# Kernel tuning notes

Hardware: AMD Instinct MI355X
Metric: run time of the kernel (lower is better)

Reference implementation:

```python
import jax, jax.numpy as jnp
import numpy as np

EMBED_DIM = 512
NUM_HEADS = 8
HEAD_DIM = EMBED_DIM // NUM_HEADS


def setup_inputs() -> dict:
    key = jax.random.key(0)
    ks = jax.random.split(key, 9)
    d = EMBED_DIM
    s = 1.0 / np.sqrt(d)
    inp = {
        "x": jax.random.normal(ks[0], (2, 4096, d), dtype=jnp.float32),
        # torch nn.Linear weights are [out, in]; we store them the same way
        "Wq": jax.random.uniform(ks[1], (d, d), jnp.float32, -s, s),
        "bq": jax.random.uniform(ks[2], (d,), jnp.float32, -s, s),
        "Wk": jax.random.uniform(ks[3], (d, d), jnp.float32, -s, s),
        "bk": jax.random.uniform(ks[4], (d,), jnp.float32, -s, s),
        "Wv": jax.random.uniform(ks[5], (d, d), jnp.float32, -s, s),
        "bv": jax.random.uniform(ks[6], (d,), jnp.float32, -s, s),
        "Wo": jax.random.uniform(ks[7], (d, d), jnp.float32, -s, s),
        "bo": jax.random.uniform(ks[8], (d,), jnp.float32, -s, s),
    }
    return inp


def reference(x, Wq, bq, Wk, bk, Wv, bv, Wo, bo):
    B, S, D = x.shape
    H, Hd = NUM_HEADS, HEAD_DIM

    def proj(W, b):  # torch Linear: x @ W.T + b
        y = jnp.einsum("bsd,ed->bse", x, W) + b
        return y.reshape(B, S, H, Hd).transpose(0, 2, 1, 3)  # [B,H,S,Hd]

    Q = proj(Wq, bq)
    K = proj(Wk, bk)
    V = proj(Wv, bv)

    scale = 1.0 / jnp.sqrt(jnp.float32(Hd))
    scores = jnp.einsum("bhqd,bhkd->bhqk", Q, K) * scale  # [B,H,S,S]
    attn = jax.nn.softmax(scores, axis=-1)
    out = jnp.einsum("bhqk,bhkd->bhqd", attn, V)  # [B,H,S,Hd]
    out = out.transpose(0, 2, 1, 3).reshape(B, S, D)
    return jnp.einsum("bsd,ed->bse", out, Wo) + bo
```

## Files before the change

kernel.cpp:

```cpp
#include <hip/hip_runtime.h>


typedef unsigned short ushortT;
typedef __attribute__((ext_vector_type(8))) short short8;
typedef __attribute__((ext_vector_type(4))) float f32x4;
typedef __attribute__((ext_vector_type(16))) float f32x16;
typedef __attribute__((ext_vector_type(4))) unsigned int uint4v;
typedef __attribute__((ext_vector_type(2))) unsigned int uint2v;

__device__ __forceinline__ ushortT f2bf(float f) {
    unsigned int u = __builtin_bit_cast(unsigned int, f);
    u += 0x7FFFu + ((u >> 16) & 1u);
    return (ushortT)(u >> 16);
}

__device__ __forceinline__ unsigned int cvtpk(float lo, float hi) {
    unsigned int d;
    asm("v_cvt_pk_bf16_f32 %0, %1, %2" : "=v"(d) : "v"(lo), "v"(hi));
    return d;
}

__device__ __forceinline__ void plswap(unsigned int &a, unsigned int &b) {
    uint2v r = __builtin_amdgcn_permlane32_swap(a, b, false, false);
    a = r[0]; b = r[1];
}

#define GLDA 40
#define ALDK 72

__device__ __forceinline__ void stage_f32(ushortT* lds, const float* src)
{
    f32x4 a0 = *(const f32x4*)(src);
    f32x4 a1 = *(const f32x4*)(src + 4);
    short8 s;
    s[0] = (short)f2bf(a0[0]); s[1] = (short)f2bf(a0[1]);
    s[2] = (short)f2bf(a0[2]); s[3] = (short)f2bf(a0[3]);
    s[4] = (short)f2bf(a1[0]); s[5] = (short)f2bf(a1[1]);
    s[6] = (short)f2bf(a1[2]); s[7] = (short)f2bf(a1[3]);
    *(short8*)lds = s;
}

__global__ __launch_bounds__(256) void proj_qkv(
    const float* __restrict__ x,
    const float* __restrict__ Wq, const float* __restrict__ bq,
    const float* __restrict__ Wk, const float* __restrict__ bk,
    const float* __restrict__ Wv, const float* __restrict__ bv,
    ushortT* __restrict__ Qw, ushortT* __restrict__ Kw,
    ushortT* __restrict__ Vtw, float qscale)
{
    __shared__ __align__(16) ushortT As[128 * GLDA];
    __shared__ __align__(16) ushortT Bs[128 * GLDA];
    const int t = threadIdx.x;
    const int w = t >> 6, lane = t & 63;
    const int quad = lane >> 4, l15 = lane & 15;
    const int z = blockIdx.z;
    const int bx = blockIdx.x, by = blockIdx.y;
    const int wm = (w >> 1) * 64, wn = (w & 1) * 64;

    const float* W    = (z == 0) ? Wq : (z == 1) ? Wk : Wv;
    const float* bias = (z == 0) ? bq : (z == 1) ? bk : bv;
    const float* Asrc = (z < 2) ? x : W;
    const float* Bsrc = (z < 2) ? W : x;
    const int arow0 = (z < 2) ? bx * 128 : by * 128;
    const int brow0 = (z < 2) ? by * 128 : bx * 128;

    f32x4 acc[4][4] = {};

    for (int k0 = 0; k0 < 512; k0 += 32) {
#pragma unroll
        for (int i = 0; i < 2; i++) {
            int c = t + i * 256;
            int row = c >> 2, cc = c & 3;
            stage_f32(As + row * GLDA + cc * 8,
                      Asrc + (size_t)(arow0 + row) * 512 + k0 + cc * 8);
            stage_f32(Bs + row * GLDA + cc * 8,
                      Bsrc + (size_t)(brow0 + row) * 512 + k0 + cc * 8);
        }
        __syncthreads();
        short8 af[4], bfr[4];
#pragma unroll
        for (int i = 0; i < 4; i++)
            af[i] = *(const short8*)(As + (wm + i * 16 + l15) * GLDA + quad * 8);
#pragma unroll
        for (int i = 0; i < 4; i++)
            bfr[i] = *(const short8*)(Bs + (wn + i * 16 + l15) * GLDA + quad * 8);
#pragma unroll
        for (int mi = 0; mi < 4; mi++)
#pragma unroll
            for (int ni = 0; ni < 4; ni++)
                acc[mi][ni] = __builtin_amdgcn_mfma_f32_16x16x32_bf16(
                    af[mi], bfr[ni], acc[mi][ni], 0, 0, 0);
        __syncthreads();
    }

    if (z < 2) {
        ushortT* Y = (z == 0) ? Qw : Kw;
        const float sc = (z == 0) ? qscale : 1.0f;
#pragma unroll
        for (int ni = 0; ni < 4; ni++) {
            int col = brow0 + wn + ni * 16 + l15;
            float bv_ = bias[col];
#pragma unroll
            for (int mi = 0; mi < 4; mi++)
#pragma unroll
                for (int r = 0; r < 4; r++) {
                    int row = arow0 + wm + mi * 16 + quad * 4 + r;
                    Y[(size_t)row * 512 + col] = f2bf((acc[mi][ni][r] + bv_) * sc);
                }
        }
    } else {
        const int bidx = brow0 >> 12;
        const int s0 = brow0 & 4095;
#pragma unroll
        for (int mi = 0; mi < 4; mi++)
#pragma unroll
            for (int r = 0; r < 4; r++) {
                int ch = arow0 + wm + mi * 16 + quad * 4 + r;
                float bv_ = bias[ch];
#pragma unroll
                for (int ni = 0; ni < 4; ni++) {
                    int s = s0 + wn + ni * 16 + l15;
                    Vtw[(size_t)bidx * 2097152 + (size_t)ch * 4096 + s] =
                        f2bf(acc[mi][ni][r] + bv_);
                }
            }
    }
}

__global__ __launch_bounds__(256) void gemm_out(
    const ushortT* __restrict__ X, const float* __restrict__ W,
    const float* __restrict__ bias, float* __restrict__ Y)
{
    __shared__ __align__(16) ushortT As[128 * GLDA];
    __shared__ __align__(16) ushortT Bs[128 * GLDA];
    const int t = threadIdx.x;
    const int w = t >> 6, lane = t & 63;
    const int quad = lane >> 4, l15 = lane & 15;
    const int bm = blockIdx.x * 128, bn = blockIdx.y * 128;
    const int wm = (w >> 1) * 64, wn = (w & 1) * 64;

    f32x4 acc[4][4] = {};

    for (int k0 = 0; k0 < 512; k0 += 32) {
#pragma unroll
        for (int i = 0; i < 2; i++) {
            int c = t + i * 256;
            int row = c >> 2, cc = c & 3;
            *(uint4v*)(As + row * GLDA + cc * 8) =
                *(const uint4v*)(X + (size_t)(bm + row) * 512 + k0 + cc * 8);
            stage_f32(Bs + row * GLDA + cc * 8,
                      W + (size_t)(bn + row) * 512 + k0 + cc * 8);
        }
        __syncthreads();
        short8 af[4], bfr[4];
#pragma unroll
        for (int i = 0; i < 4; i++)
            af[i] = *(const short8*)(As + (wm + i * 16 + l15) * GLDA + quad * 8);
#pragma unroll
        for (int i = 0; i < 4; i++)
            bfr[i] = *(const short8*)(Bs + (wn + i * 16 + l15) * GLDA + quad * 8);
#pragma unroll
        for (int mi = 0; mi < 4; mi++)
#pragma unroll
            for (int ni = 0; ni < 4; ni++)
                acc[mi][ni] = __builtin_amdgcn_mfma_f32_16x16x32_bf16(
                    af[mi], bfr[ni], acc[mi][ni], 0, 0, 0);
        __syncthreads();
    }

#pragma unroll
    for (int ni = 0; ni < 4; ni++) {
        int col = bn + wn + ni * 16 + l15;
        float bv = bias[col];
#pragma unroll
        for (int mi = 0; mi < 4; mi++)
#pragma unroll
            for (int r = 0; r < 4; r++) {
                int row = bm + wm + mi * 16 + quad * 4 + r;
                Y[(size_t)row * 512 + col] = acc[mi][ni][r] + bv;
            }
    }
}

__global__ __launch_bounds__(512) void attn(
    const ushortT* Q, const ushortT* __restrict__ K,
    const ushortT* __restrict__ Vt, ushortT* O)
{
    __shared__ __align__(16) ushortT Ks[2][2][64 * ALDK];
    __shared__ __align__(16) ushortT Vs[2][2][64 * ALDK];

    const int t = threadIdx.x;
    const int w = t >> 6, lane = t & 63;
    const int half = w >> 2, wq = w & 3;
    const int l31 = lane & 31, hh = lane >> 5;
    const int qt = blockIdx.x, bh = blockIdx.y;
    const int b = bh >> 3, h = bh & 7;
    const size_t qrow = (size_t)b * 4096 + qt * 128 + wq * 32 + l31;

    short8 qf[4];
    {
        const ushortT* qp = Q + qrow * 512 + h * 64 + hh * 8;
#pragma unroll
        for (int dk = 0; dk < 4; dk++)
            qf[dk] = *(const short8*)(qp + dk * 16);
    }

    f32x16 oacc[2] = {};
    float lpart = 0.f;

    const int kofs = half * 2048;
    const ushortT* Kbase = K + ((size_t)b * 4096 + kofs) * 512 + h * 64;
    const ushortT* Vbase = Vt + (size_t)b * 2097152 + (size_t)h * 64 * 4096 + kofs;

    const int th = t & 255;
    const int srow = th >> 3, scol = (th & 7) * 8;
    uint4v kg[2], vg[2];

#pragma unroll
    for (int i = 0; i < 2; i++) {
        kg[i] = *(const uint4v*)(Kbase + (size_t)(srow + 32 * i) * 512 + scol);
        vg[i] = *(const uint4v*)(Vbase + (size_t)(srow + 32 * i) * 4096 + scol);
    }
#pragma unroll
    for (int i = 0; i < 2; i++) {
        *(uint4v*)(Ks[half][0] + (srow + 32 * i) * ALDK + scol) = kg[i];
        *(uint4v*)(Vs[half][0] + (srow + 32 * i) * ALDK + scol) = vg[i];
    }
    __syncthreads();

    for (int kt = 0; kt < 32; kt++) {
        const int cur = kt & 1;

        if (kt < 31) {
            const int kb = (kt + 1) * 64;
#pragma unroll
            for (int i = 0; i < 2; i++) {
                kg[i] = *(const uint4v*)(Kbase + (size_t)(kb + srow + 32 * i) * 512 + scol);
                vg[i] = *(const uint4v*)(Vbase + (size_t)(srow + 32 * i) * 4096 + kb + scol);
            }
        }

        const ushortT* Kt = Ks[half][cur];
        const ushortT* Vtl = Vs[half][cur];

#pragma unroll
        for (int st = 0; st < 2; st++) {
            f32x16 sacc = {};
#pragma unroll
            for (int dk = 0; dk < 4; dk++) {
                short8 kf = *(const short8*)(Kt + (st * 32 + l31) * ALDK + dk * 16 + hh * 8);
                sacc = __builtin_amdgcn_mfma_f32_32x32x16_bf16(kf, qf[dk], sacc, 0, 0, 0);
            }
            float p[16];
#pragma unroll
            for (int r = 0; r < 16; r++) {
                p[r] = __builtin_amdgcn_exp2f(sacc[r]);
                lpart += p[r];
            }
            unsigned int c00 = cvtpk(p[0],  p[1]),  c01 = cvtpk(p[2],  p[3]);
            unsigned int c10 = cvtpk(p[4],  p[5]),  c11 = cvtpk(p[6],  p[7]);
            unsigned int c20 = cvtpk(p[8],  p[9]),  c21 = cvtpk(p[10], p[11]);
            unsigned int c30 = cvtpk(p[12], p[13]), c31 = cvtpk(p[14], p[15]);
            plswap(c00, c10);
            plswap(c01, c11);
            plswap(c20, c30);
            plswap(c21, c31);
            uint4v b0v = { c00, c01, c10, c11 };
            uint4v b1v = { c20, c21, c30, c31 };
            short8 B0 = __builtin_bit_cast(short8, b0v);
            short8 B1 = __builtin_bit_cast(short8, b1v);

#pragma unroll
            for (int dt = 0; dt < 2; dt++) {
                short8 vf0 = *(const short8*)(Vtl + (dt * 32 + l31) * ALDK + st * 32 + hh * 8);
                short8 vf1 = *(const short8*)(Vtl + (dt * 32 + l31) * ALDK + st * 32 + 16 + hh * 8);
                oacc[dt] = __builtin_amdgcn_mfma_f32_32x32x16_bf16(vf0, B0, oacc[dt], 0, 0, 0);
                oacc[dt] = __builtin_amdgcn_mfma_f32_32x32x16_bf16(vf1, B1, oacc[dt], 0, 0, 0);
            }
        }

        if (kt < 31) {
            const int nb = cur ^ 1;
#pragma unroll
            for (int i = 0; i < 2; i++) {
                *(uint4v*)(Ks[half][nb] + (srow + 32 * i) * ALDK + scol) = kg[i];
                *(uint4v*)(Vs[half][nb] + (srow + 32 * i) * ALDK + scol) = vg[i];
            }
        }
        __syncthreads();
    }

    float* scratch = (float*)&Ks[0][0][0];
    float* prow = scratch + (size_t)(wq * 64 + lane) * 36;

    if (half == 1) {
#pragma unroll
        for (int dt = 0; dt < 2; dt++)
#pragma unroll
            for (int m = 0; m < 4; m++) {
                f32x4 v4 = { oacc[dt][4 * m + 0], oacc[dt][4 * m + 1],
                             oacc[dt][4 * m + 2], oacc[dt][4 * m + 3] };
                *(f32x4*)(prow + dt * 16 + m * 4) = v4;
            }
        prow[32] = lpart;
    }
    __syncthreads();

    if (half == 0) {
        float sum = lpart + prow[32];
        float l = sum + __shfl_xor(sum, 32);
        float rl = 1.0f / l;

        ushortT* orow = O + qrow * 512 + h * 64 + hh * 4;
#pragma unroll
        for (int dt = 0; dt < 2; dt++)
#pragma unroll
            for (int m = 0; m < 4; m++) {
                f32x4 v4 = *(const f32x4*)(prow + dt * 16 + m * 4);
                unsigned int u0 = cvtpk((oacc[dt][4 * m + 0] + v4[0]) * rl,
                                        (oacc[dt][4 * m + 1] + v4[1]) * rl);
                unsigned int u1 = cvtpk((oacc[dt][4 * m + 2] + v4[2]) * rl,
                                        (oacc[dt][4 * m + 3] + v4[3]) * rl);
                uint2v st2 = { u0, u1 };
                *(uint2v*)(orow + dt * 32 + m * 8) = st2;
            }
    }
}

extern "C" void kernel_launch(void* const* d_in, const int* in_sizes, int n_in,
                              void* d_out, int out_size, void* d_ws, size_t ws_size,
                              hipStream_t stream)
{
    const float* x  = (const float*)d_in[0];
    const float* Wq = (const float*)d_in[1];
    const float* bq = (const float*)d_in[2];
    const float* Wk = (const float*)d_in[3];
    const float* bk = (const float*)d_in[4];
    const float* Wv = (const float*)d_in[5];
    const float* bv = (const float*)d_in[6];
    const float* Wo = (const float*)d_in[7];
    const float* bo = (const float*)d_in[8];

    ushortT* ws  = (ushortT*)d_ws;
    ushortT* Qw  = ws;
    ushortT* Kw  = ws + 4194304;
    ushortT* Vtw = ws + 2 * 4194304;

    const float qscale = 0.125f * 1.44269504089f;

    proj_qkv<<<dim3(64, 4, 3), 256, 0, stream>>>(
        x, Wq, bq, Wk, bk, Wv, bv, Qw, Kw, Vtw, qscale);
    attn<<<dim3(32, 16), 512, 0, stream>>>(Qw, Kw, Vtw, Qw);
    gemm_out<<<dim3(64, 4), 256, 0, stream>>>(Qw, Wo, bo, (float*)d_out);
}
```

Measured before the change: 218.6 us.

## Double query rows per attention wave and register-prefetch GEMM staging loads

The attention kernel now gives each wave 64 query rows (two 32-row groups), so every K/V fragment read from LDS feeds twice as many MFMAs, and the grid is halved to 16x16 blocks. Launch bounds are set to request two blocks per CU, and the merge scratch is widened to hold both groups. The projection and output GEMMs prefetch the next k-tile's global loads into registers while the current tile computes, and use packed bf16 conversion instructions instead of scalar rounding. The costs are much higher register pressure in attention, possible spills or lower occupancy, and only 256 attention blocks, which may underfill the GPU.

```diff
diff --git a/kernel.cpp b/kernel.cpp
--- a/kernel.cpp
+++ b/kernel.cpp
@@ -20,6 +20,12 @@
     return d;
 }
 
+__device__ __forceinline__ uint4v pk8(f32x4 a0, f32x4 a1) {
+    uint4v r = { cvtpk(a0[0], a0[1]), cvtpk(a0[2], a0[3]),
+                 cvtpk(a1[0], a1[1]), cvtpk(a1[2], a1[3]) };
+    return r;
+}
+
 __device__ __forceinline__ void plswap(unsigned int &a, unsigned int &b) {
     uint2v r = __builtin_amdgcn_permlane32_swap(a, b, false, false);
     a = r[0]; b = r[1];
@@ -27,18 +33,6 @@
 
 #define GLDA 40
 #define ALDK 72
-
-__device__ __forceinline__ void stage_f32(ushortT* lds, const float* src)
-{
-    f32x4 a0 = *(const f32x4*)(src);
-    f32x4 a1 = *(const f32x4*)(src + 4);
-    short8 s;
-    s[0] = (short)f2bf(a0[0]); s[1] = (short)f2bf(a0[1]);
-    s[2] = (short)f2bf(a0[2]); s[3] = (short)f2bf(a0[3]);
-    s[4] = (short)f2bf(a1[0]); s[5] = (short)f2bf(a1[1]);
-    s[6] = (short)f2bf(a1[2]); s[7] = (short)f2bf(a1[3]);
-    *(short8*)lds = s;
-}
 
 __global__ __launch_bounds__(256) void proj_qkv(
     const float* __restrict__ x,
@@ -64,19 +58,42 @@
     const int arow0 = (z < 2) ? bx * 128 : by * 128;
     const int brow0 = (z < 2) ? by * 128 : bx * 128;
 
+    const int sr0 = t >> 2, sc0 = (t & 3) * 8;
+    const int sr1 = (t + 256) >> 2, sc1 = ((t + 256) & 3) * 8;
+
+    f32x4 pa[2][2], pb[2][2];
+    {
+        const float* ap0 = Asrc + (size_t)(arow0 + sr0) * 512 + sc0;
+        const float* ap1 = Asrc + (size_t)(arow0 + sr1) * 512 + sc1;
+        const float* bp0 = Bsrc + (size_t)(brow0 + sr0) * 512 + sc0;
+        const float* bp1 = Bsrc + (size_t)(brow0 + sr1) * 512 + sc1;
+        pa[0][0] = *(const f32x4*)ap0; pa[0][1] = *(const f32x4*)(ap0 + 4);
+        pa[1][0] = *(const f32x4*)ap1; pa[1][1] = *(const f32x4*)(ap1 + 4);
+        pb[0][0] = *(const f32x4*)bp0; pb[0][1] = *(const f32x4*)(bp0 + 4);
+        pb[1][0] = *(const f32x4*)bp1; pb[1][1] = *(const f32x4*)(bp1 + 4);
+    }
+
     f32x4 acc[4][4] = {};
 
     for (int k0 = 0; k0 < 512; k0 += 32) {
-#pragma unroll
-        for (int i = 0; i < 2; i++) {
-            int c = t + i * 256;
-            int row = c >> 2, cc = c & 3;
-            stage_f32(As + row * GLDA + cc * 8,
-                      Asrc + (size_t)(arow0 + row) * 512 + k0 + cc * 8);
-            stage_f32(Bs + row * GLDA + cc * 8,
-                      Bsrc + (size_t)(brow0 + row) * 512 + k0 + cc * 8);
-        }
+        *(uint4v*)(As + sr0 * GLDA + sc0) = pk8(pa[0][0], pa[0][1]);
+        *(uint4v*)(As + sr1 * GLDA + sc1) = pk8(pa[1][0], pa[1][1]);
+        *(uint4v*)(Bs + sr0 * GLDA + sc0) = pk8(pb[0][0], pb[0][1]);
+        *(uint4v*)(Bs + sr1 * GLDA + sc1) = pk8(pb[1][0], pb[1][1]);
         __syncthreads();
+
+        if (k0 < 480) {
+            const int kn = k0 + 32;
+            const float* ap0 = Asrc + (size_t)(arow0 + sr0) * 512 + kn + sc0;
+            const float* ap1 = Asrc + (size_t)(arow0 + sr1) * 512 + kn + sc1;
+            const float* bp0 = Bsrc + (size_t)(brow0 + sr0) * 512 + kn + sc0;
+            const float* bp1 = Bsrc + (size_t)(brow0 + sr1) * 512 + kn + sc1;
+            pa[0][0] = *(const f32x4*)ap0; pa[0][1] = *(const f32x4*)(ap0 + 4);
+            pa[1][0] = *(const f32x4*)ap1; pa[1][1] = *(const f32x4*)(ap1 + 4);
+            pb[0][0] = *(const f32x4*)bp0; pb[0][1] = *(const f32x4*)(bp0 + 4);
+            pb[1][0] = *(const f32x4*)bp1; pb[1][1] = *(const f32x4*)(bp1 + 4);
+        }
+
         short8 af[4], bfr[4];
 #pragma unroll
         for (int i = 0; i < 4; i++)
@@ -139,19 +156,39 @@
     const int bm = blockIdx.x * 128, bn = blockIdx.y * 128;
     const int wm = (w >> 1) * 64, wn = (w & 1) * 64;
 
+    const int sr0 = t >> 2, sc0 = (t & 3) * 8;
+    const int sr1 = (t + 256) >> 2, sc1 = ((t + 256) & 3) * 8;
+
+    uint4v pa[2];
+    f32x4 pb[2][2];
+    {
+        pa[0] = *(const uint4v*)(X + (size_t)(bm + sr0) * 512 + sc0);
+        pa[1] = *(const uint4v*)(X + (size_t)(bm + sr1) * 512 + sc1);
+        const float* bp0 = W + (size_t)(bn + sr0) * 512 + sc0;
+        const float* bp1 = W + (size_t)(bn + sr1) * 512 + sc1;
+        pb[0][0] = *(const f32x4*)bp0; pb[0][1] = *(const f32x4*)(bp0 + 4);
+        pb[1][0] = *(const f32x4*)bp1; pb[1][1] = *(const f32x4*)(bp1 + 4);
+    }
+
     f32x4 acc[4][4] = {};
 
     for (int k0 = 0; k0 < 512; k0 += 32) {
-#pragma unroll
-        for (int i = 0; i < 2; i++) {
-            int c = t + i * 256;
-            int row = c >> 2, cc = c & 3;
-            *(uint4v*)(As + row * GLDA + cc * 8) =
-                *(const uint4v*)(X + (size_t)(bm + row) * 512 + k0 + cc * 8);
-            stage_f32(Bs + row * GLDA + cc * 8,
-                      W + (size_t)(bn + row) * 512 + k0 + cc * 8);
-        }
+        *(uint4v*)(As + sr0 * GLDA + sc0) = pa[0];
+        *(uint4v*)(As + sr1 * GLDA + sc1) = pa[1];
+        *(uint4v*)(Bs + sr0 * GLDA + sc0) = pk8(pb[0][0], pb[0][1]);
+        *(uint4v*)(Bs + sr1 * GLDA + sc1) = pk8(pb[1][0], pb[1][1]);
         __syncthreads();
+
+        if (k0 < 480) {
+            const int kn = k0 + 32;
+            pa[0] = *(const uint4v*)(X + (size_t)(bm + sr0) * 512 + kn + sc0);
+            pa[1] = *(const uint4v*)(X + (size_t)(bm + sr1) * 512 + kn + sc1);
+            const float* bp0 = W + (size_t)(bn + sr0) * 512 + kn + sc0;
+            const float* bp1 = W + (size_t)(bn + sr1) * 512 + kn + sc1;
+            pb[0][0] = *(const f32x4*)bp0; pb[0][1] = *(const f32x4*)(bp0 + 4);
+            pb[1][0] = *(const f32x4*)bp1; pb[1][1] = *(const f32x4*)(bp1 + 4);
+        }
+
         short8 af[4], bfr[4];
 #pragma unroll
         for (int i = 0; i < 4; i++)
@@ -182,31 +219,52 @@
     }
 }
 
-__global__ __launch_bounds__(512) void attn(
+__device__ __forceinline__ void softmax_pack(const f32x16 &sacc, float &lp,
+                                             uint4v &B0, uint4v &B1)
+{
+    float p[16];
+#pragma unroll
+    for (int r = 0; r < 16; r++) {
+        p[r] = __builtin_amdgcn_exp2f(sacc[r]);
+        lp += p[r];
+    }
+    unsigned int c00 = cvtpk(p[0],  p[1]),  c01 = cvtpk(p[2],  p[3]);
+    unsigned int c10 = cvtpk(p[4],  p[5]),  c11 = cvtpk(p[6],  p[7]);
+    unsigned int c20 = cvtpk(p[8],  p[9]),  c21 = cvtpk(p[10], p[11]);
+    unsigned int c30 = cvtpk(p[12], p[13]), c31 = cvtpk(p[14], p[15]);
+    plswap(c00, c10);
+    plswap(c01, c11);
+    plswap(c20, c30);
+    plswap(c21, c31);
+    B0 = uint4v{ c00, c01, c10, c11 };
+    B1 = uint4v{ c20, c21, c30, c31 };
+}
+
+__global__ __launch_bounds__(512, 2) void attn(
     const ushortT* Q, const ushortT* __restrict__ K,
     const ushortT* __restrict__ Vt, ushortT* O)
 {
-    __shared__ __align__(16) ushortT Ks[2][2][64 * ALDK];
-    __shared__ __align__(16) ushortT Vs[2][2][64 * ALDK];
+    __shared__ __align__(16) ushortT SM[2][2][2][64 * ALDK];
 
     const int t = threadIdx.x;
     const int w = t >> 6, lane = t & 63;
-    const int half = w >> 2, wq = w & 3;
+    const int half = w >> 2, qw = w & 3;
     const int l31 = lane & 31, hh = lane >> 5;
     const int qt = blockIdx.x, bh = blockIdx.y;
     const int b = bh >> 3, h = bh & 7;
-    const size_t qrow = (size_t)b * 4096 + qt * 128 + wq * 32 + l31;
-
-    short8 qf[4];
-    {
-        const ushortT* qp = Q + qrow * 512 + h * 64 + hh * 8;
+    const size_t qbase = (size_t)b * 4096 + qt * 256 + qw * 64;
+
+    short8 qf[2][4];
+#pragma unroll
+    for (int qg = 0; qg < 2; qg++) {
+        const ushortT* qp = Q + (qbase + qg * 32 + l31) * 512 + h * 64 + hh * 8;
 #pragma unroll
         for (int dk = 0; dk < 4; dk++)
-            qf[dk] = *(const short8*)(qp + dk * 16);
-    }
-
-    f32x16 oacc[2] = {};
-    float lpart = 0.f;
+            qf[qg][dk] = *(const short8*)(qp + dk * 16);
+    }
+
+    f32x16 oacc[2][2] = {};
+    float lpart[2] = {};
 
     const int kofs = half * 2048;
     const ushortT* Kbase = K + ((size_t)b * 4096 + kofs) * 512 + h * 64;
@@ -223,8 +281,8 @@
     }
 #pragma unroll
     for (int i = 0; i < 2; i++) {
-        *(uint4v*)(Ks[half][0] + (srow + 32 * i) * ALDK + scol) = kg[i];
-        *(uint4v*)(Vs[half][0] + (srow + 32 * i) * ALDK + scol) = vg[i];
+        *(uint4v*)(SM[0][half][0] + (srow + 32 * i) * ALDK + scol) = kg[i];
+        *(uint4v*)(SM[1][half][0] + (srow + 32 * i) * ALDK + scol) = vg[i];
     }
     __syncthreads();
 
@@ -240,42 +298,38 @@
             }
         }
 
-        const ushortT* Kt = Ks[half][cur];
-        const ushortT* Vtl = Vs[half][cur];
+        const ushortT* Kt  = SM[0][half][cur];
+        const ushortT* Vtl = SM[1][half][cur];
 
 #pragma unroll
         for (int st = 0; st < 2; st++) {
-            f32x16 sacc = {};
+            short8 kf[4];
+#pragma unroll
+            for (int dk = 0; dk < 4; dk++)
+                kf[dk] = *(const short8*)(Kt + (st * 32 + l31) * ALDK + dk * 16 + hh * 8);
+            f32x16 s0 = {}, s1 = {};
 #pragma unroll
             for (int dk = 0; dk < 4; dk++) {
-                short8 kf = *(const short8*)(Kt + (st * 32 + l31) * ALDK + dk * 16 + hh * 8);
-                sacc = __builtin_amdgcn_mfma_f32_32x32x16_bf16(kf, qf[dk], sacc, 0, 0, 0);
-            }
-            float p[16];
-#pragma unroll
-            for (int r = 0; r < 16; r++) {
-                p[r] = __builtin_amdgcn_exp2f(sacc[r]);
-                lpart += p[r];
-            }
-            unsigned int c00 = cvtpk(p[0],  p[1]),  c01 = cvtpk(p[2],  p[3]);
-            unsigned int c10 = cvtpk(p[4],  p[5]),  c11 = cvtpk(p[6],  p[7]);
-            unsigned int c20 = cvtpk(p[8],  p[9]),  c21 = cvtpk(p[10], p[11]);
-            unsigned int c30 = cvtpk(p[12], p[13]), c31 = cvtpk(p[14], p[15]);
-            plswap(c00, c10);
-            plswap(c01, c11);
-            plswap(c20, c30);
-            plswap(c21, c31);
-            uint4v b0v = { c00, c01, c10, c11 };
-            uint4v b1v = { c20, c21, c30, c31 };
-            short8 B0 = __builtin_bit_cast(short8, b0v);
-            short8 B1 = __builtin_bit_cast(short8, b1v);
+                s0 = __builtin_amdgcn_mfma_f32_32x32x16_bf16(kf[dk], qf[0][dk], s0, 0, 0, 0);
+                s1 = __builtin_amdgcn_mfma_f32_32x32x16_bf16(kf[dk], qf[1][dk], s1, 0, 0, 0);
+            }
+
+            uint4v B00, B01, B10, B11;
+            softmax_pack(s0, lpart[0], B00, B01);
+            softmax_pack(s1, lpart[1], B10, B11);
+            short8 p00 = __builtin_bit_cast(short8, B00);
+            short8 p01 = __builtin_bit_cast(short8, B01);
+            short8 p10 = __builtin_bit_cast(short8, B10);
+            short8 p11 = __builtin_bit_cast(short8, B11);
 
 #pragma unroll
             for (int dt = 0; dt < 2; dt++) {
                 short8 vf0 = *(const short8*)(Vtl + (dt * 32 + l31) * ALDK + st * 32 + hh * 8);
                 short8 vf1 = *(const short8*)(Vtl + (dt * 32 + l31) * ALDK + st * 32 + 16 + hh * 8);
-                oacc[dt] = __builtin_amdgcn_mfma_f32_32x32x16_bf16(vf0, B0, oacc[dt], 0, 0, 0);
-                oacc[dt] = __builtin_amdgcn_mfma_f32_32x32x16_bf16(vf1, B1, oacc[dt], 0, 0, 0);
+                oacc[0][dt] = __builtin_amdgcn_mfma_f32_32x32x16_bf16(vf0, p00, oacc[0][dt], 0, 0, 0);
+                oacc[0][dt] = __builtin_amdgcn_mfma_f32_32x32x16_bf16(vf1, p01, oacc[0][dt], 0, 0, 0);
+                oacc[1][dt] = __builtin_amdgcn_mfma_f32_32x32x16_bf16(vf0, p10, oacc[1][dt], 0, 0, 0);
+                oacc[1][dt] = __builtin_amdgcn_mfma_f32_32x32x16_bf16(vf1, p11, oacc[1][dt], 0, 0, 0);
             }
         }
 
@@ -283,47 +337,53 @@
             const int nb = cur ^ 1;
 #pragma unroll
             for (int i = 0; i < 2; i++) {
-                *(uint4v*)(Ks[half][nb] + (srow + 32 * i) * ALDK + scol) = kg[i];
-                *(uint4v*)(Vs[half][nb] + (srow + 32 * i) * ALDK + scol) = vg[i];
+                *(uint4v*)(SM[0][half][nb] + (srow + 32 * i) * ALDK + scol) = kg[i];
+                *(uint4v*)(SM[1][half][nb] + (srow + 32 * i) * ALDK + scol) = vg[i];
             }
         }
         __syncthreads();
     }
 
-    float* scratch = (float*)&Ks[0][0][0];
-    float* prow = scratch + (size_t)(wq * 64 + lane) * 36;
+    float* scratch = (float*)&SM[0][0][0][0];
+    float* prow = scratch + (size_t)(qw * 64 + lane) * 68;
 
     if (half == 1) {
 #pragma unroll
-        for (int dt = 0; dt < 2; dt++)
-#pragma unroll
-            for (int m = 0; m < 4; m++) {
-                f32x4 v4 = { oacc[dt][4 * m + 0], oacc[dt][4 * m + 1],
-                             oacc[dt][4 * m + 2], oacc[dt][4 * m + 3] };
-                *(f32x4*)(prow + dt * 16 + m * 4) = v4;
-            }
-        prow[32] = lpart;
+        for (int qg = 0; qg < 2; qg++)
+#pragma unroll
+            for (int dt = 0; dt < 2; dt++)
+#pragma unroll
+                for (int m = 0; m < 4; m++) {
+                    f32x4 v4 = { oacc[qg][dt][4 * m + 0], oacc[qg][dt][4 * m + 1],
+                                 oacc[qg][dt][4 * m + 2], oacc[qg][dt][4 * m + 3] };
+                    *(f32x4*)(prow + qg * 32 + dt * 16 + m * 4) = v4;
+                }
+        prow[64] = lpart[0];
+        prow[65] = lpart[1];
     }
     __syncthreads();
 
     if (half == 0) {
-        float sum = lpart + prow[32];
-        float l = sum + __shfl_xor(sum, 32);
-        float rl = 1.0f / l;
-
-        ushortT* orow = O + qrow * 512 + h * 64 + hh * 4;
-#pragma unroll
-        for (int dt = 0; dt < 2; dt++)
-#pragma unroll
-            for (int m = 0; m < 4; m++) {
-                f32x4 v4 = *(const f32x4*)(prow + dt * 16 + m * 4);
-                unsigned int u0 = cvtpk((oacc[dt][4 * m + 0] + v4[0]) * rl,
-                                        (oacc[dt][4 * m + 1] + v4[1]) * rl);
-                unsigned int u1 = cvtpk((oacc[dt][4 * m + 2] + v4[2]) * rl,
-                                        (oacc[dt][4 * m + 3] + v4[3]) * rl);
-                uint2v st2 = { u0, u1 };
-                *(uint2v*)(orow + dt * 32 + m * 8) = st2;
-            }
+#pragma unroll
+        for (int qg = 0; qg < 2; qg++) {
+            float sum = lpart[qg] + prow[64 + qg];
+            float l = sum + __shfl_xor(sum, 32);
+            float rl = 1.0f / l;
+
+            ushortT* orow = O + (qbase + qg * 32 + l31) * 512 + h * 64 + hh * 4;
+#pragma unroll
+            for (int dt = 0; dt < 2; dt++)
+#pragma unroll
+                for (int m = 0; m < 4; m++) {
+                    f32x4 v4 = *(const f32x4*)(prow + qg * 32 + dt * 16 + m * 4);
+                    unsigned int u0 = cvtpk((oacc[qg][dt][4 * m + 0] + v4[0]) * rl,
+                                            (oacc[qg][dt][4 * m + 1] + v4[1]) * rl);
+                    unsigned int u1 = cvtpk((oacc[qg][dt][4 * m + 2] + v4[2]) * rl,
+                                            (oacc[qg][dt][4 * m + 3] + v4[3]) * rl);
+                    uint2v st2 = { u0, u1 };
+                    *(uint2v*)(orow + dt * 32 + m * 8) = st2;
+                }
+        }
     }
 }
 
@@ -350,6 +410,6 @@
 
     proj_qkv<<<dim3(64, 4, 3), 256, 0, stream>>>(
         x, Wq, bq, Wk, bk, Wv, bv, Qw, Kw, Vtw, qscale);
-    attn<<<dim3(32, 16), 512, 0, stream>>>(Qw, Kw, Vtw, Qw);
+    attn<<<dim3(16, 16), 512, 0, stream>>>(Qw, Kw, Vtw, Qw);
     gemm_out<<<dim3(64, 4), 256, 0, stream>>>(Qw, Wo, bo, (float*)d_out);
 }
```

After: 189.6 us. 13.3% less time.
